# Performance work log

Hardware: AMD Instinct MI355X
Metric: run time of the kernel (lower is better)

Reference implementation:

```python
import jax, jax.numpy as jnp
import numpy as np

ROPE_BASE = 10000.0

def _rope(x, positions):
    # x: [B, H, T, hs], rotate-half (GPT-NeoX style) rotary embedding
    hs = x.shape[-1]
    half = hs // 2
    inv_freq = 1.0 / (ROPE_BASE ** (jnp.arange(half, dtype=jnp.float32) / half))
    ang = positions.astype(jnp.float32)[:, None] * inv_freq[None, :]  # [T, half]
    cos, sin = jnp.cos(ang), jnp.sin(ang)
    x1, x2 = x[..., :half], x[..., half:]
    return jnp.concatenate([x1 * cos - x2 * sin, x1 * sin + x2 * cos], axis=-1)


def setup_inputs() -> dict:
    key = jax.random.key(0)
    ks = jax.random.split(key, 8)
    B, T, OFF, C, H = 1, 1024, 1024, 2048, 16
    hs = C // H
    return {
        "x": jax.random.normal(ks[0], (B, T, C), jnp.float32),
        "cached_k": jax.random.normal(ks[1], (B, H, OFF, hs), jnp.float32),
        "cached_v": jax.random.normal(ks[2], (B, H, OFF, hs), jnp.float32),
        "W_attn": jax.random.normal(ks[3], (C, 3 * C), jnp.float32) * 0.02,
        "b_attn": jnp.zeros((3 * C,), jnp.float32),
        "W_proj": jax.random.normal(ks[4], (C, C), jnp.float32) * 0.02,
        "b_proj": jnp.zeros((C,), jnp.float32),
        "decay_raw": jax.random.normal(ks[5], (16,), jnp.float32) * 0.5,
    }


def reference(x, cached_k, cached_v, W_attn, b_attn, W_proj, b_proj, decay_raw):
    B, T, C = x.shape
    H = decay_raw.shape[0]
    hs = C // H
    off = cached_k.shape[2]

    qkv = x @ W_attn + b_attn                       # [B, T, 3C]
    q, k, v = jnp.split(qkv, 3, axis=-1)
    to_heads = lambda t: t.reshape(B, T, H, hs).transpose(0, 2, 1, 3)  # [B,H,T,hs]
    q, k, v = to_heads(q), to_heads(k), to_heads(v)

    positions = jnp.arange(off, off + T)
    q = _rope(q, positions)
    k = _rope(k, positions)

    k = jnp.concatenate([cached_k, k], axis=2)      # [B, H, T_full, hs]
    v = jnp.concatenate([cached_v, v], axis=2)
    T_full = k.shape[2]

    # causal mask over full key length, offset for cache
    neg_inf = jnp.finfo(jnp.float32).min
    q_idx = positions                               # [T]
    k_idx = jnp.arange(T_full)                      # [T_full]
    causal = jnp.where(k_idx[None, :] > q_idx[:, None], neg_inf, 0.0)  # [T, T_full]

    # per-head distance-decay log-bias
    decay = jax.nn.softplus(decay_raw)              # [H]
    dist = jnp.maximum(q_idx[:, None] - k_idx[None, :], 0).astype(jnp.float32)
    logw = -jnp.log1p(decay[:, None, None] * jnp.log1p(dist))          # [H, T, T_full]
    bias = causal[None, :, :] + logw                # [H, T, T_full]

    scale = 1.0 / jnp.sqrt(jnp.float32(hs))
    scores = jnp.einsum('bhtd,bhsd->bhts', q, k) * scale + bias[None]
    attn = jax.nn.softmax(scores, axis=-1)
    y = jnp.einsum('bhts,bhsd->bhtd', attn, v)      # [B, H, T, hs]
    y = y.transpose(0, 2, 1, 3).reshape(B, T, C)
    y = y @ W_proj + b_proj
    return (y, k, v)
```

## Files before the change

kernel.cpp:

```cpp
#include <hip/hip_runtime.h>
#include <hip/hip_bf16.h>

typedef unsigned short u16;
typedef unsigned int u32;
typedef __attribute__((ext_vector_type(4))) float f32x4;
typedef float f32x4u __attribute__((ext_vector_type(4), aligned(4)));
typedef __attribute__((ext_vector_type(8))) short bf16x8;

__device__ __forceinline__ u16 f2bf(float f) {
    union { float f; u32 u; } v; v.f = f;
    return (u16)((v.u + 0x7FFFu + ((v.u >> 16) & 1u)) >> 16);
}
__device__ __forceinline__ float bf2f(u16 b) {
    union { u32 u; float f; } v; v.u = ((u32)b) << 16;
    return v.f;
}
__device__ __forceinline__ void st_out(float* p, float v) { *p = v; }
__device__ __forceinline__ void st_out(u16* p, float v) { *p = f2bf(v); }

__device__ __forceinline__ f32x4 mfma16(bf16x8 a, bf16x8 b, f32x4 c) {
    return __builtin_amdgcn_mfma_f32_16x16x32_bf16(a, b, c, 0, 0, 0);
}
__device__ __forceinline__ u32 cvt_pk_bf16(float lo, float hi) {
    u32 r;
    asm("v_cvt_pk_bf16_f32 %0, %1, %2" : "=v"(r) : "v"(lo), "v"(hi));
    return r;
}

#define GLD_LDS16(g, l) __builtin_amdgcn_global_load_lds( \
    (const __attribute__((address_space(1))) void*)(g),   \
    (__attribute__((address_space(3))) void*)(l), 16, 0, 0)

#define LOG2E 1.4426950408889634f
#define QSCALE 0.12751743f

__global__ __launch_bounds__(256) void k_prep(
    const float* __restrict__ W_attn, const float* __restrict__ W_proj,
    const float* __restrict__ x, const float* __restrict__ decay_raw,
    u16* __restrict__ WaT, u16* __restrict__ WpT, u16* __restrict__ Xb,
    float* __restrict__ bias_tab, float* __restrict__ cosT, float* __restrict__ sinT) {
    __shared__ float tile[64][65];
    const int b = blockIdx.x, tid = threadIdx.x;
    if (b < 4096) {
        const float* src; u16* dst; int R, Cc, bx, by;
        if (b < 3072) { src = W_attn; dst = WaT; R = 2048; Cc = 6144; bx = b % 96; by = b / 96; }
        else          { src = W_proj; dst = WpT; R = 2048; Cc = 2048; bx = (b - 3072) & 31; by = (b - 3072) >> 5; }
        int c0 = bx * 64, r0 = by * 64;
#pragma unroll
        for (int it = 0; it < 16; ++it) {
            int idx = it * 256 + tid;
            int r = idx >> 6, c = idx & 63;
            tile[r][c] = src[(size_t)(r0 + r) * Cc + c0 + c];
        }
        __syncthreads();
#pragma unroll
        for (int it = 0; it < 16; ++it) {
            int idx = it * 256 + tid;
            int cc = idx >> 6, rr = idx & 63;
            dst[(size_t)(c0 + cc) * R + r0 + rr] = f2bf(tile[rr][cc]);
        }
    } else if (b < 6144) {
        int i = (b - 4096) * 256 + tid;
        float4 v = ((const float4*)x)[i];
        u32 p0 = (u32)f2bf(v.x) | ((u32)f2bf(v.y) << 16);
        u32 p1 = (u32)f2bf(v.z) | ((u32)f2bf(v.w) << 16);
        uint2 p; p.x = p0; p.y = p1;
        *(uint2*)(Xb + (size_t)i * 4) = p;
    } else {
        int i = (b - 6144) * 256 + tid;
        if (i < 16 * 2048) {
            int h = i >> 11, dist = i & 2047;
            float dec = log1pf(expf(decay_raw[h]));
            bias_tab[i] = -log1pf(dec * log1pf((float)dist)) * LOG2E;
        }
        if (i < 1024 * 64) {
            int t = i >> 6, j = i & 63;
            float inv = expf(-logf(10000.0f) * (float)j / 64.0f);
            float ang = (float)(1024 + t) * inv;
            cosT[i] = cosf(ang);
            sinT[i] = sinf(ang);
        }
    }
}

template<int BM, int BN, int WRG, int WCG, typename OT>
__global__ __launch_bounds__(256) void k_gemm_bt(
    const u16* __restrict__ A, const u16* __restrict__ Bt,
    const float* __restrict__ bias, OT* __restrict__ C,
    int M, int N, int K) {
    constexpr int BK = 64;
    constexpr int WM = BM / WRG;
    constexpr int WN = BN / WCG;
    constexpr int MR = WM / 16;
    constexpr int NR = WN / 16;
    constexpr int LDSZ = (BM + BN) * BK * 2;
    __shared__ char lds[2][LDSZ];

    const int tid = threadIdx.x;
    const int lane = tid & 63, wid = tid >> 6;
    const int wr = wid / WCG, wc = wid % WCG;
    const int lhi = lane >> 4, llo = lane & 15;
    const int m0 = blockIdx.y * BM, n0 = blockIdx.x * BN;

    f32x4 acc[MR][NR];
#pragma unroll
    for (int m = 0; m < MR; ++m)
#pragma unroll
        for (int n = 0; n < NR; ++n)
            acc[m][n] = f32x4{0.f, 0.f, 0.f, 0.f};

    auto stage = [&](int buf, int k0) {
        char* ldsA = &lds[buf][0];
        char* ldsB = &lds[buf][0] + BM * BK * 2;
#pragma unroll
        for (int it = 0; it < (BM * 8) / 256; ++it) {
            int ci = it * 256 + wid * 64 + lane;
            int r = ci >> 3, c = ci & 7;
            int sc = c ^ (r & 7);
            GLD_LDS16(A + (size_t)(m0 + r) * K + k0 + sc * 8,
                      ldsA + (it * 256 + wid * 64) * 16);
        }
#pragma unroll
        for (int it = 0; it < (BN * 8) / 256; ++it) {
            int ci = it * 256 + wid * 64 + lane;
            int r = ci >> 3, c = ci & 7;
            int sc = c ^ (r & 7);
            GLD_LDS16(Bt + (size_t)(n0 + r) * K + k0 + sc * 8,
                      ldsB + (it * 256 + wid * 64) * 16);
        }
    };

    stage(0, 0);
    __syncthreads();
    int cur = 0;
    for (int k0 = 0; k0 < K; k0 += BK) {
        if (k0 + BK < K) stage(cur ^ 1, k0 + BK);
        const char* ldsA = &lds[cur][0];
        const char* ldsB = &lds[cur][0] + BM * BK * 2;
#pragma unroll
        for (int kk = 0; kk < BK; kk += 32) {
            bf16x8 af[MR], bfr[NR];
            const int clb = (kk >> 3) + lhi;
#pragma unroll
            for (int m = 0; m < MR; ++m) {
                int row = wr * WM + m * 16 + llo;
                af[m] = *(const bf16x8*)(ldsA + row * 128 + ((clb ^ (row & 7)) << 4));
            }
#pragma unroll
            for (int n = 0; n < NR; ++n) {
                int row = wc * WN + n * 16 + llo;
                bfr[n] = *(const bf16x8*)(ldsB + row * 128 + ((clb ^ (row & 7)) << 4));
            }
#pragma unroll
            for (int m = 0; m < MR; ++m)
#pragma unroll
                for (int n = 0; n < NR; ++n)
                    acc[m][n] = mfma16(af[m], bfr[n], acc[m][n]);
        }
        __syncthreads();
        cur ^= 1;
    }
#pragma unroll
    for (int m = 0; m < MR; ++m) {
        int row = m0 + wr * WM + m * 16 + lhi * 4;
#pragma unroll
        for (int n = 0; n < NR; ++n) {
            int col = n0 + wc * WN + n * 16 + llo;
            float bv = bias[col];
#pragma unroll
            for (int j = 0; j < 4; ++j)
                st_out(&C[(size_t)(row + j) * N + col], acc[m][n][j] + bv);
        }
    }
}

__global__ void k_fuse2(const u16* __restrict__ qkv,
                        const float* __restrict__ cosT, const float* __restrict__ sinT,
                        const float* __restrict__ cached_k,
                        u16* __restrict__ qb, u16* __restrict__ kb,
                        float* __restrict__ out_k) {
    const int b = blockIdx.x;
    if (b < 4096) {
        int i = b * 256 + threadIdx.x;
        int j = i & 63;
        int t = (i >> 6) & 1023;
        int h = i >> 16;
        const u16* row = qkv + (size_t)t * 6144;
        float q1 = bf2f(row[h * 128 + j]),        q2 = bf2f(row[h * 128 + j + 64]);
        float k1 = bf2f(row[2048 + h * 128 + j]), k2 = bf2f(row[2048 + h * 128 + j + 64]);
        float cv = cosT[t * 64 + j], sv = sinT[t * 64 + j];
        float qo1 = q1 * cv - q2 * sv, qo2 = q1 * sv + q2 * cv;
        float ko1 = k1 * cv - k2 * sv, ko2 = k1 * sv + k2 * cv;
        size_t qoff = ((size_t)h * 1024 + t) * 128 + j;
        qb[qoff] = f2bf(qo1 * QSCALE); qb[qoff + 64] = f2bf(qo2 * QSCALE);
        size_t koff = ((size_t)h * 2048 + 1024 + t) * 128 + j;
        kb[koff] = f2bf(ko1); kb[koff + 64] = f2bf(ko2);
        out_k[koff] = ko1; out_k[koff + 64] = ko2;
    } else {
        int i = (b - 4096) * 256 + threadIdx.x;
        int d = i & 127, s = (i >> 7) & 1023, h = i >> 17;
        float v = cached_k[i];
        size_t off = ((size_t)h * 2048 + s) * 128 + d;
        out_k[off] = v;
        kb[off] = f2bf(v);
    }
}

__global__ __launch_bounds__(256) void k_v_assemble(
    const float* __restrict__ cached_v, const u16* __restrict__ qkv,
    float* __restrict__ out_v, u16* __restrict__ vt) {
    __shared__ u16 tile[64][65];
    int s0 = blockIdx.x * 64, d0 = blockIdx.y * 64, h = blockIdx.z;
    int tid = threadIdx.x;
#pragma unroll
    for (int it = 0; it < 16; ++it) {
        int idx = it * 256 + tid;
        int r = idx >> 6, c = idx & 63;
        int s = s0 + r, d = d0 + c;
        u16 v = (s < 1024)
            ? f2bf(cached_v[((size_t)h * 1024 + s) * 128 + d])
            : qkv[(size_t)(s - 1024) * 6144 + 4096 + h * 128 + d];
        tile[r][c] = v;
        out_v[((size_t)h * 2048 + s) * 128 + d] = bf2f(v);
    }
    __syncthreads();
#pragma unroll
    for (int it = 0; it < 16; ++it) {
        int idx = it * 256 + tid;
        int dd = idx >> 6, ss = idx & 63;
        vt[((size_t)h * 128 + d0 + dd) * 2048 + s0 + ss] = tile[ss][dd];
    }
}

__global__ __launch_bounds__(256, 4) void k_attn(
    const u16* __restrict__ qb,
    const u16* __restrict__ kb,
    const u16* __restrict__ vt,
    const float* __restrict__ bias_tab,
    u16* __restrict__ Pacc,
    float* __restrict__ Pm,
    float* __restrict__ Pl) {
    __shared__ char ldsK[2][32 * 256];
    __shared__ char ldsV[2][128 * 64];

    const int bid = blockIdx.x;
    const int xcd = bid & 7, idx = bid >> 3;
    const int work = xcd * 128 + idx;
    const int h = work >> 6, rem = work & 63;
    const int qt = rem >> 2, chunk = rem & 3;
    const int qbase = qt * 64;
    const int tid = threadIdx.x, lane = tid & 63, wid = tid >> 6;
    const int lhi = lane >> 4, llo = lane & 15;
    const int slot = (h * 16 + qt) * 4 + chunk;

    const u16* kg = kb + (size_t)h * 2048 * 128;
    const u16* vg = vt + (size_t)h * 128 * 2048;
    const float* bt = bias_tab + h * 2048;

    bf16x8 qf[4];
    {
        const u16* qrow = qb + ((size_t)h * 1024 + qbase + wid * 16 + llo) * 128;
#pragma unroll
        for (int c = 0; c < 4; ++c)
            qf[c] = *(const bf16x8*)(qrow + c * 32 + lhi * 8);
    }

    f32x4 acc[8];
#pragma unroll
    for (int d = 0; d < 8; ++d) acc[d] = f32x4{0.f, 0.f, 0.f, 0.f};
    float mrow = -3e38f;
    float lrow = 0.f;

    const int ntiles = 34 + 2 * qt;
    const int qpos = 1024 + qbase + wid * 16 + llo;

    auto stage = [&](int b, int st) {
        int sbase = st * 32;
#pragma unroll
        for (int it = 0; it < 2; ++it) {
            int ci = it * 256 + tid;
            int r = ci >> 4, c = ci & 15;
            int sc = c ^ (r & 7);
            GLD_LDS16(kg + (size_t)(sbase + r) * 128 + sc * 8,
                      &ldsK[b][0] + (it * 256 + wid * 64) * 16);
        }
#pragma unroll
        for (int it = 0; it < 2; ++it) {
            int ci = it * 256 + tid;
            int r = ci >> 2, c = ci & 3;
            int sc = c ^ ((r >> 1) & 3);
            GLD_LDS16(vg + (size_t)r * 2048 + sbase + sc * 8,
                      &ldsV[b][0] + (it * 256 + wid * 64) * 16);
        }
    };

    auto permP = [&](u32 p0, u32 p1, u32 p2, u32 p3) -> bf16x8 {
        u32 r16a = (u32)__shfl_xor((int)(lhi == 1 ? p0 : p2), 16);
        u32 r16b = (u32)__shfl_xor((int)(lhi == 1 ? p1 : p3), 16);
        u32 r32a = (u32)__shfl_xor((int)(lhi == 3 ? p0 : p2), 32);
        u32 r32b = (u32)__shfl_xor((int)(lhi == 3 ? p1 : p3), 32);
        u32 r48a = (u32)__shfl_xor((int)(lhi == 2 ? p0 : p2), 48);
        u32 r48b = (u32)__shfl_xor((int)(lhi == 2 ? p1 : p3), 48);
        union { u32 w[4]; bf16x8 v; } u;
        u.w[0] = lhi == 0 ? p0 : lhi == 1 ? r48a : lhi == 2 ? r32a : r16a;
        u.w[1] = lhi == 0 ? p1 : lhi == 1 ? r48b : lhi == 2 ? r32b : r16b;
        u.w[2] = lhi == 0 ? r16a : lhi == 1 ? r32a : lhi == 2 ? r48a : p2;
        u.w[3] = lhi == 0 ? r16b : lhi == 1 ? r32b : lhi == 2 ? r48b : p3;
        return u.v;
    };

    const int st0 = chunk + 4 * ((ntiles - 1 - chunk) >> 2);
    stage(0, st0);
    __syncthreads();
    int cur = 0;
    for (int st = st0; st >= chunk; st -= 4) {
        if (st >= chunk + 4) stage(cur ^ 1, st - 4);
        const int sbase = st * 32;
        const char* lK = &ldsK[cur][0];
        const char* lV = &ldsV[cur][0];

        const int D0 = qpos - sbase - lhi * 4;
        f32x4u wB = *(const f32x4u*)(bt + (D0 - 3 < 0 ? 0 : D0 - 3));
        f32x4u wC = *(const f32x4u*)(bt + (D0 - 19 < 0 ? 0 : D0 - 19));

        f32x4 sc4[2];
        __builtin_amdgcn_s_setprio(1);
#pragma unroll
        for (int sub = 0; sub < 2; ++sub) {
            f32x4 s4 = f32x4{0.f, 0.f, 0.f, 0.f};
            int key = sub * 16 + llo;
#pragma unroll
            for (int c2 = 0; c2 < 4; ++c2) {
                int cl = c2 * 4 + lhi;
                bf16x8 kf = *(const bf16x8*)(lK + key * 256 + ((cl ^ (key & 7)) << 4));
                s4 = mfma16(kf, qf[c2], s4);
            }
            sc4[sub] = s4;
        }
        __builtin_amdgcn_s_setprio(0);

        if (sbase + 31 <= 1024 + qbase + wid * 16) {
#pragma unroll
            for (int j = 0; j < 4; ++j) {
                sc4[0][j] += wB[3 - j];
                sc4[1][j] += wC[3 - j];
            }
        } else {
#pragma unroll
            for (int sub = 0; sub < 2; ++sub)
#pragma unroll
                for (int j = 0; j < 4; ++j) {
                    int key = sbase + sub * 16 + lhi * 4 + j;
                    int dist = qpos - key;
                    float bv = bt[dist < 0 ? 0 : dist];
                    sc4[sub][j] = (dist < 0) ? -3e38f : sc4[sub][j] + bv;
                }
        }

        float tmax = fmaxf(fmaxf(fmaxf(sc4[0][0], sc4[0][1]), fmaxf(sc4[0][2], sc4[0][3])),
                           fmaxf(fmaxf(sc4[1][0], sc4[1][1]), fmaxf(sc4[1][2], sc4[1][3])));
        int ok = (tmax <= mrow + 11.5416f) ? 1 : 0;
        if (!__all(ok)) {
            float t = tmax;
            t = fmaxf(t, __shfl_xor(t, 16));
            t = fmaxf(t, __shfl_xor(t, 32));
            float mnew = fmaxf(mrow, t);
            float fs = exp2f(mrow - mnew);
            mrow = mnew;
            lrow *= fs;
            float fsj[4];
#pragma unroll
            for (int j = 0; j < 4; ++j)
                fsj[j] = __shfl(fs, lhi * 4 + j);
#pragma unroll
            for (int d = 0; d < 8; ++d)
#pragma unroll
                for (int j = 0; j < 4; ++j) acc[d][j] *= fsj[j];
        }

        float p[8];
#pragma unroll
        for (int sub = 0; sub < 2; ++sub)
#pragma unroll
            for (int j = 0; j < 4; ++j) {
                float e = exp2f(sc4[sub][j] - mrow);
                lrow += e;
                p[sub * 4 + j] = e;
            }
        bf16x8 pa = permP(cvt_pk_bf16(p[0], p[1]), cvt_pk_bf16(p[2], p[3]),
                          cvt_pk_bf16(p[4], p[5]), cvt_pk_bf16(p[6], p[7]));

        __builtin_amdgcn_s_setprio(1);
#pragma unroll
        for (int db = 0; db < 8; ++db) {
            int dr = db * 16 + llo;
            int cl = lhi ^ ((dr >> 1) & 3);
            bf16x8 vf = *(const bf16x8*)(lV + dr * 64 + cl * 16);
            acc[db] = mfma16(pa, vf, acc[db]);
        }
        __builtin_amdgcn_s_setprio(0);
        __syncthreads();
        cur ^= 1;
    }

    {
        float t = lrow;
        t += __shfl_xor(t, 16);
        t += __shfl_xor(t, 32);
        lrow = t;
    }

    if (lhi == 0) {
        int r = wid * 16 + llo;
        Pm[(size_t)slot * 64 + r] = mrow;
        Pl[(size_t)slot * 64 + r] = lrow;
    }
#pragma unroll
    for (int db = 0; db < 8; ++db)
#pragma unroll
        for (int j = 0; j < 4; ++j) {
            int r = wid * 16 + lhi * 4 + j;
            Pacc[(size_t)slot * 8192 + r * 128 + db * 16 + llo] = f2bf(acc[db][j]);
        }
}

__global__ __launch_bounds__(256) void k_merge(
    const u16* __restrict__ Pacc, const float* __restrict__ Pm,
    const float* __restrict__ Pl, u16* __restrict__ yb) {
    const int b = blockIdx.x;
    const int h = b >> 6, qt = (b >> 2) & 15, quarter = b & 3;
    const int slot0 = (h * 16 + qt) * 4;
    const int tid = threadIdx.x;
    const int r = tid >> 2, dd = (tid & 3) * 8 + quarter * 32;

    float m[4], l[4];
#pragma unroll
    for (int c = 0; c < 4; ++c) {
        m[c] = Pm[(size_t)(slot0 + c) * 64 + r];
        l[c] = Pl[(size_t)(slot0 + c) * 64 + r];
    }
    float M = fmaxf(fmaxf(m[0], m[1]), fmaxf(m[2], m[3]));
    float w[4], L = 0.f;
#pragma unroll
    for (int c = 0; c < 4; ++c) {
        w[c] = exp2f(m[c] - M);
        L += w[c] * l[c];
    }
    float inv = 1.0f / L;

    float y[8];
#pragma unroll
    for (int i = 0; i < 8; ++i) y[i] = 0.f;
#pragma unroll
    for (int c = 0; c < 4; ++c) {
        const uint4* pa = (const uint4*)(Pacc + (size_t)(slot0 + c) * 8192 + r * 128 + dd);
        float wc = w[c];
        uint4 v = *pa;
        u32 a[4] = {v.x, v.y, v.z, v.w};
#pragma unroll
        for (int p = 0; p < 4; ++p) {
            y[p * 2]     += wc * bf2f((u16)(a[p] & 0xFFFF));
            y[p * 2 + 1] += wc * bf2f((u16)(a[p] >> 16));
        }
    }
    int trow = qt * 64 + r;
    uint4 outv;
    u32* ow = (u32*)&outv;
#pragma unroll
    for (int k = 0; k < 4; ++k)
        ow[k] = (u32)f2bf(y[2 * k] * inv) | ((u32)f2bf(y[2 * k + 1] * inv) << 16);
    *(uint4*)(yb + (size_t)trow * 2048 + h * 128 + dd) = outv;
}

extern "C" void kernel_launch(void* const* d_in, const int* in_sizes, int n_in,
                              void* d_out, int out_size, void* d_ws, size_t ws_size,
                              hipStream_t stream) {
    (void)in_sizes; (void)n_in; (void)out_size;
    const float* x         = (const float*)d_in[0];
    const float* cached_k  = (const float*)d_in[1];
    const float* cached_v  = (const float*)d_in[2];
    const float* W_attn    = (const float*)d_in[3];
    const float* b_attn    = (const float*)d_in[4];
    const float* W_proj    = (const float*)d_in[5];
    const float* b_proj    = (const float*)d_in[6];
    const float* decay_raw = (const float*)d_in[7];

    float* out_y = (float*)d_out;
    float* out_k = out_y + 2097152;
    float* out_v = out_y + 6291456;

    char* ws = (char*)d_ws;
    if (ws_size < 63569920) return;
    u16*   WaT  = (u16*)(ws);
    u16*   WpT  = (u16*)(ws + 25165824);
    u16*   Xb   = (u16*)(ws + 33554432);
    u16*   QKVb = (u16*)(ws + 37748736);
    float* BT   = (float*)(ws + 62914560);
    float* CT   = (float*)(ws + 63045632);
    float* ST   = (float*)(ws + 63307776);
    u16*   Qb   = (u16*)(ws);
    u16*   Kb   = (u16*)(ws + 4194304);
    u16*   Vt   = (u16*)(ws + 12582912);
    u16*   Yb   = (u16*)(ws + 20971520);
    float* Pm   = (float*)(ws + 33554432);
    float* Pl   = (float*)(ws + 33816576);
    u16*   Pacc = (u16*)(ws + 37748736);

    k_prep<<<6400, 256, 0, stream>>>(W_attn, W_proj, x, decay_raw, WaT, WpT, Xb, BT, CT, ST);
    k_gemm_bt<128, 64, 2, 2, u16><<<dim3(96, 8), 256, 0, stream>>>(Xb, WaT, b_attn, QKVb, 1024, 6144, 2048);
    k_fuse2<<<12288, 256, 0, stream>>>(QKVb, CT, ST, cached_k, Qb, Kb, out_k);
    k_v_assemble<<<dim3(32, 2, 16), 256, 0, stream>>>(cached_v, QKVb, out_v, Vt);
    k_attn<<<1024, 256, 0, stream>>>(Qb, Kb, Vt, BT, Pacc, Pm, Pl);
    k_merge<<<1024, 256, 0, stream>>>(Pacc, Pm, Pl, Yb);
    k_gemm_bt<64, 64, 2, 2, float><<<dim3(32, 16), 256, 0, stream>>>(Yb, WpT, b_proj, out_y, 1024, 2048, 2048);
}
```

Measured before the change: 135.3 us.

## Use explicit vmcnt waits in GEMM, reverse query-tile order, tweak softmax rescale

The GEMM main loop swaps __syncthreads for explicit s_waitcnt vmcnt plus raw s_barrier with sched barriers. This lets the next stage's global-to-LDS loads stay in flight while the current tile is computed. The attention kernel reverses query-tile order so heavier causal tiles start first, and lowers the lazy-rescale threshold. The row sum is also accumulated from the bf16-rounded probabilities, so it matches the values fed to the MFMA. Relying on vmcnt counts assumes a fixed number of loads per stage, which the compiler must not change.

```diff
diff --git a/kernel.cpp b/kernel.cpp
--- a/kernel.cpp
+++ b/kernel.cpp
@@ -25,6 +25,11 @@
     u32 r;
     asm("v_cvt_pk_bf16_f32 %0, %1, %2" : "=v"(r) : "v"(lo), "v"(hi));
     return r;
+}
+template<int N> __device__ __forceinline__ void wait_vmcnt() {
+    if constexpr (N == 0) asm volatile("s_waitcnt vmcnt(0)" ::: "memory");
+    else if constexpr (N == 4) asm volatile("s_waitcnt vmcnt(4)" ::: "memory");
+    else if constexpr (N == 6) asm volatile("s_waitcnt vmcnt(6)" ::: "memory");
 }
 
 #define GLD_LDS16(g, l) __builtin_amdgcn_global_load_lds( \
@@ -94,6 +99,7 @@
     constexpr int MR = WM / 16;
     constexpr int NR = WN / 16;
     constexpr int LDSZ = (BM + BN) * BK * 2;
+    constexpr int NLOAD = (BM + BN) * 8 / 256;
     __shared__ char lds[2][LDSZ];
 
     const int tid = threadIdx.x;
@@ -131,10 +137,17 @@
     };
 
     stage(0, 0);
-    __syncthreads();
     int cur = 0;
     for (int k0 = 0; k0 < K; k0 += BK) {
-        if (k0 + BK < K) stage(cur ^ 1, k0 + BK);
+        if (k0 + BK < K) {
+            stage(cur ^ 1, k0 + BK);
+            wait_vmcnt<NLOAD>();
+        } else {
+            wait_vmcnt<0>();
+        }
+        __builtin_amdgcn_s_barrier();
+        __builtin_amdgcn_sched_barrier(0);
+        asm volatile("" ::: "memory");
         const char* ldsA = &lds[cur][0];
         const char* ldsB = &lds[cur][0] + BM * BK * 2;
 #pragma unroll
@@ -157,7 +170,11 @@
                 for (int n = 0; n < NR; ++n)
                     acc[m][n] = mfma16(af[m], bfr[n], acc[m][n]);
         }
-        __syncthreads();
+        asm volatile("" ::: "memory");
+        __builtin_amdgcn_sched_barrier(0);
+        __builtin_amdgcn_s_barrier();
+        __builtin_amdgcn_sched_barrier(0);
+        asm volatile("" ::: "memory");
         cur ^= 1;
     }
 #pragma unroll
@@ -247,7 +264,7 @@
     const int xcd = bid & 7, idx = bid >> 3;
     const int work = xcd * 128 + idx;
     const int h = work >> 6, rem = work & 63;
-    const int qt = rem >> 2, chunk = rem & 3;
+    const int qt = 15 - (rem >> 2), chunk = rem & 3;
     const int qbase = qt * 64;
     const int tid = threadIdx.x, lane = tid & 63, wid = tid >> 6;
     const int lhi = lane >> 4, llo = lane & 15;
@@ -359,7 +376,7 @@
 
         float tmax = fmaxf(fmaxf(fmaxf(sc4[0][0], sc4[0][1]), fmaxf(sc4[0][2], sc4[0][3])),
                            fmaxf(fmaxf(sc4[1][0], sc4[1][1]), fmaxf(sc4[1][2], sc4[1][3])));
-        int ok = (tmax <= mrow + 11.5416f) ? 1 : 0;
+        int ok = (tmax <= mrow + 8.0f) ? 1 : 0;
         if (!__all(ok)) {
             float t = tmax;
             t = fmaxf(t, __shfl_xor(t, 16));
@@ -382,13 +399,15 @@
 #pragma unroll
         for (int sub = 0; sub < 2; ++sub)
 #pragma unroll
-            for (int j = 0; j < 4; ++j) {
-                float e = exp2f(sc4[sub][j] - mrow);
-                lrow += e;
-                p[sub * 4 + j] = e;
-            }
-        bf16x8 pa = permP(cvt_pk_bf16(p[0], p[1]), cvt_pk_bf16(p[2], p[3]),
-                          cvt_pk_bf16(p[4], p[5]), cvt_pk_bf16(p[6], p[7]));
+            for (int j = 0; j < 4; ++j)
+                p[sub * 4 + j] = exp2f(sc4[sub][j] - mrow);
+        u32 pk0 = cvt_pk_bf16(p[0], p[1]), pk1 = cvt_pk_bf16(p[2], p[3]);
+        u32 pk2 = cvt_pk_bf16(p[4], p[5]), pk3 = cvt_pk_bf16(p[6], p[7]);
+        lrow += bf2f((u16)(pk0 & 0xFFFF)) + bf2f((u16)(pk0 >> 16))
+              + bf2f((u16)(pk1 & 0xFFFF)) + bf2f((u16)(pk1 >> 16))
+              + bf2f((u16)(pk2 & 0xFFFF)) + bf2f((u16)(pk2 >> 16))
+              + bf2f((u16)(pk3 & 0xFFFF)) + bf2f((u16)(pk3 >> 16));
+        bf16x8 pa = permP(pk0, pk1, pk2, pk3);
 
         __builtin_amdgcn_s_setprio(1);
 #pragma unroll
```

Result: no change. 133.4 us (-1.4%).
